# Optimization experiments

Hardware: AMD Instinct MI355X
Metric: run time of the kernel (lower is better)

## Reference

```python
import jax, jax.numpy as jnp
import numpy as np

WS = 7      # window size
NH = 4      # num heads
SHIFT = 3   # cyclic shift

def _rel_index():
    coords = np.stack(np.meshgrid(np.arange(WS), np.arange(WS), indexing='ij')).reshape(2, -1)
    rel = (coords[:, :, None] - coords[:, None, :]).transpose(1, 2, 0).astype(np.int64)
    rel[..., 0] += WS - 1
    rel[..., 1] += WS - 1
    rel[..., 0] *= 2 * WS - 1
    return rel.sum(-1)  # (49, 49)

_REL_IDX = _rel_index()

def _ln(x, g, b):
    mu = x.mean(-1, keepdims=True)
    var = ((x - mu) ** 2).mean(-1, keepdims=True)
    return (x - mu) / jnp.sqrt(var + 1e-5) * g + b

def setup_inputs() -> dict:
    key = jax.random.key(0)
    ks = jax.random.split(key, 8)
    B, H, W, C, HID = 64, 56, 56, 128, 512
    s = 0.02
    return {
        'x': jax.random.normal(ks[0], (B, H * W, C), jnp.float32),
        'norm1_g': jnp.ones((C,), jnp.float32),
        'norm1_b': jnp.zeros((C,), jnp.float32),
        'qkv_w': jax.random.normal(ks[1], (3 * C, C), jnp.float32) * s,
        'qkv_b': jax.random.normal(ks[2], (3 * C,), jnp.float32) * s,
        'proj_w': jax.random.normal(ks[3], (C, C), jnp.float32) * s,
        'proj_b': jax.random.normal(ks[4], (C,), jnp.float32) * s,
        'rpb_table': jax.random.normal(ks[5], ((2 * WS - 1) ** 2, NH), jnp.float32) * s,
        'norm2_g': jnp.ones((C,), jnp.float32),
        'norm2_b': jnp.zeros((C,), jnp.float32),
        'fc1_w': jax.random.normal(ks[6], (HID, C), jnp.float32) * s,
        'fc1_b': jnp.zeros((HID,), jnp.float32),
        'fc2_w': jax.random.normal(ks[7], (C, HID), jnp.float32) * s,
        'fc2_b': jnp.zeros((C,), jnp.float32),
        'H': H,
        'W': W,
    }

def reference(x, norm1_g, norm1_b, qkv_w, qkv_b, proj_w, proj_b, rpb_table,
              norm2_g, norm2_b, fc1_w, fc1_b, fc2_w, fc2_b, H, W):
    B, L, C = x.shape
    hd = C // NH
    scale = hd ** (-0.5)
    shortcut = x
    h = _ln(x, norm1_g, norm1_b).reshape(B, H, W, C)
    pad_h = (-H) % WS
    pad_w = (-W) % WS
    if pad_h or pad_w:
        h = jnp.pad(h, ((0, 0), (0, pad_h), (0, pad_w), (0, 0)))
    Hp, Wp = H + pad_h, W + pad_w
    if SHIFT > 0:
        h = jnp.roll(h, (-SHIFT, -SHIFT), axis=(1, 2))
    # window partition -> (B*nW, 49, C)
    h = h.reshape(B, Hp // WS, WS, Wp // WS, WS, C).transpose(0, 1, 3, 2, 4, 5).reshape(-1, WS * WS, C)
    qkv = h @ qkv_w.T + qkv_b  # (nW, 49, 3C)
    q, k, v = [t.reshape(-1, WS * WS, NH, hd).transpose(0, 2, 1, 3) for t in jnp.split(qkv, 3, axis=-1)]
    attn = jnp.einsum('whnd,whmd->whnm', q * scale, k)  # (nW, NH, 49, 49)
    bias = rpb_table[_REL_IDX.reshape(-1)].reshape(WS * WS, WS * WS, NH).transpose(2, 0, 1)
    attn = jax.nn.softmax(attn + bias[None], axis=-1)
    o = jnp.einsum('whnm,whmd->whnd', attn, v).transpose(0, 2, 1, 3).reshape(-1, WS * WS, C)
    o = o @ proj_w.T + proj_b
    # window reverse -> (B, Hp, Wp, C)
    o = o.reshape(B, Hp // WS, Wp // WS, WS, WS, C).transpose(0, 1, 3, 2, 4, 5).reshape(B, Hp, Wp, C)
    if SHIFT > 0:
        o = jnp.roll(o, (SHIFT, SHIFT), axis=(1, 2))
    o = o[:, :H, :W].reshape(B, H * W, C)
    x = shortcut + o
    h2 = _ln(x, norm2_g, norm2_b)
    h2 = jax.nn.gelu(h2 @ fc1_w.T + fc1_b, approximate=False)
    return x + (h2 @ fc2_w.T + fc2_b)
```

## Files before the change

### kernel.cpp

```cpp
#include <hip/hip_runtime.h>
#include <stdint.h>

static constexpr int Bz   = 64;
static constexpr int HH   = 56, WWp = 56;
static constexpr int C    = 128, HID = 512;
static constexpr int L    = HH * WWp;
static constexpr int M    = Bz * L;
static constexpr int NWIN = Bz * 64;
static constexpr int NH   = 4;
static constexpr int SHIFT = 3;

typedef __bf16 bf16x8 __attribute__((ext_vector_type(8)));
typedef float  f32x4  __attribute__((ext_vector_type(4)));

__device__ __forceinline__ float bf2f(unsigned short u) {
    return __uint_as_float(((unsigned int)u) << 16);
}
__device__ __forceinline__ unsigned short f2bf(float f) {
    unsigned int u = __float_as_uint(f);
    return (unsigned short)((u + 0x7FFFu + ((u >> 16) & 1u)) >> 16);
}
__device__ __forceinline__ unsigned pkbf(float a, float b) {
    unsigned r;
    asm("v_cvt_pk_bf16_f32 %0, %1, %2" : "=v"(r) : "v"(a), "v"(b));
    return r;
}
__device__ __forceinline__ unsigned lds_addr(const void* p) {
    return (unsigned)(size_t)(__attribute__((address_space(3))) const char*)p;
}
__device__ __forceinline__ float gelu_s(float x) {
    float e = __expf(-1.702f * x);
    return x * __builtin_amdgcn_rcpf(1.0f + e);
}

__device__ __forceinline__ int win2orig(int m) {
    int w = m / 49, t = m - w * 49;
    int b = w >> 6, wi = (w >> 3) & 7, wj = w & 7;
    int ti = t / 7, tj = t - ti * 7;
    int i = wi * 7 + ti + SHIFT; if (i >= HH) i -= HH;
    int j = wj * 7 + tj + SHIFT; if (j >= WWp) j -= WWp;
    return b * L + i * WWp + j;
}

__device__ __forceinline__ void async_copy16(void* ldsdst, const void* gsrc) {
    __builtin_amdgcn_global_load_lds(
        (const __attribute__((address_space(1))) unsigned int*)gsrc,
        (__attribute__((address_space(3))) unsigned int*)ldsdst,
        16, 0, 0);
}

__global__ __launch_bounds__(256) void wconv_kernel(
    const float* __restrict__ qkvw, const float* __restrict__ projw,
    const float* __restrict__ fc1w, const float* __restrict__ fc2w,
    const float* __restrict__ rpb, float* __restrict__ biasd,
    unsigned short* __restrict__ wb) {
    int i = blockIdx.x * 256 + threadIdx.x;
    float v;
    if (i < 49152)       v = qkvw[i];
    else if (i < 65536)  v = projw[i - 49152];
    else if (i < 131072) v = fc1w[i - 65536];
    else                 v = fc2w[i - 131072];
    wb[i] = f2bf(v);
    if (i < 16384) {
        int h = i >> 12, l = (i >> 6) & 63, f = i & 63;
        int mi = f >> 4, ni = (f >> 2) & 3, r = f & 3;
        int ii = mi * 16 + (l >> 4) * 4 + r;
        int jj = ni * 16 + (l & 15);
        float bv;
        if (jj >= 49)      bv = -1e30f;
        else if (ii >= 49) bv = 0.f;
        else {
            int yi = ii / 7, xi = ii - yi * 7, yj = jj / 7, xj = jj - yj * 7;
            bv = rpb[((yi - yj + 6) * 13 + (xi - xj + 6)) * NH + h];
        }
        biasd[i] = bv;
    }
}

__global__ __launch_bounds__(256) void ln_kernel(const float* __restrict__ in,
                                                 const float* __restrict__ g,
                                                 const float* __restrict__ bta,
                                                 unsigned short* __restrict__ out) {
    int row  = blockIdx.x * 4 + (threadIdx.x >> 6);
    int lane = threadIdx.x & 63;
    const float2 v = ((const float2*)(in + (long)row * C))[lane];
    float s  = v.x + v.y;
    float ss = v.x * v.x + v.y * v.y;
#pragma unroll
    for (int off = 32; off >= 1; off >>= 1) {
        s  += __shfl_xor(s, off);
        ss += __shfl_xor(ss, off);
    }
    float mu  = s * (1.0f / C);
    float var = ss * (1.0f / C) - mu * mu;
    float rs  = rsqrtf(var + 1e-5f);
    float2 gg = ((const float2*)g)[lane];
    float2 bb = ((const float2*)bta)[lane];
    unsigned o = pkbf((v.x - mu) * rs * gg.x + bb.x,
                      (v.y - mu) * rs * gg.y + bb.y);
    ((unsigned*)(out + (long)row * C))[lane] = o;
}

template<int MODE, int K, int NB, bool GATHER>
__global__ __launch_bounds__(256) void gemm_pipe(
    const unsigned short* __restrict__ A,
    const unsigned short* __restrict__ Wb,
    const float* __restrict__ bias,
    const float* __restrict__ residf,
    const unsigned short* __restrict__ residb,
    const float* __restrict__ g2, const float* __restrict__ b2,
    float* __restrict__ outf,
    unsigned short* __restrict__ outb,
    unsigned short* __restrict__ outb2)
{
    constexpr int KH = K / 64;
    __shared__ char lds[65536];
    char* ldsA = lds;
    char* ldsB = lds + 32768;
    const int tid = threadIdx.x;
    const int wid = tid >> 6, lane = tid & 63;
    const int g = lane >> 4, lr = lane & 15;
    const int wm = wid >> 1, wn = wid & 1;
    const int mbase = blockIdx.x * 128;

    auto stageAfull = [&]() {
#pragma unroll
        for (int i = 0; i < 8; ++i) {
            const int c = i * 4 + wid;
            const int r = (c << 2) + (lane >> 4);
            const int s = (lane & 15) ^ (r & 15);
            long arow = GATHER ? (long)win2orig(mbase + r) : (long)(mbase + r);
            async_copy16(ldsA + c * 1024, (const char*)A + arow * (K * 2) + s * 16);
        }
    };
    auto stageBhalf = [&](int buf, int nb, int kh) {
#pragma unroll
        for (int i = 0; i < 4; ++i) {
            const int c = i * 4 + wid;
            const int r = (c << 3) + (lane >> 3);
            const int s = (lane & 7) ^ (r & 7);
            async_copy16(ldsB + buf * 16384 + c * 1024,
                         (const char*)Wb + (long)(nb * 128 + r) * (K * 2) + kh * 128 + s * 16);
        }
    };

    stageAfull();
    stageBhalf(0, 0, 0);
    __syncthreads();
    int cur = 0;

    for (int nb = 0; nb < NB; ++nb) {
        f32x4 acc[4][4] = {};
        for (int kh = 0; kh < KH; ++kh) {
            const bool last = (nb == NB - 1) && (kh == KH - 1);
            if (!last) {
                const int nnb = (kh == KH - 1) ? nb + 1 : nb;
                const int nkh = (kh == KH - 1) ? 0 : kh + 1;
                stageBhalf(cur ^ 1, nnb, nkh);
            }
#pragma unroll
            for (int kkh = 0; kkh < 2; ++kkh) {
                bf16x8 af[4], bfr[4];
#pragma unroll
                for (int mi = 0; mi < 4; ++mi) {
                    const int ra = wm * 64 + mi * 16 + lr;
                    const int kk = kh * 2 + kkh;
                    af[mi] = *(const bf16x8*)(ldsA + ra * 256 + (((kk * 4 + g) ^ (ra & 15)) * 16));
                }
#pragma unroll
                for (int ni = 0; ni < 4; ++ni) {
                    const int rb = wn * 64 + ni * 16 + lr;
                    bfr[ni] = *(const bf16x8*)(ldsB + cur * 16384 + rb * 128 + (((kkh * 4 + g) ^ (rb & 7)) * 16));
                }
#pragma unroll
                for (int mi = 0; mi < 4; ++mi)
#pragma unroll
                    for (int ni = 0; ni < 4; ++ni)
                        acc[mi][ni] = __builtin_amdgcn_mfma_f32_16x16x32_bf16(bfr[ni], af[mi], acc[mi][ni], 0, 0, 0);
            }
            if (!last) { __syncthreads(); cur ^= 1; }
        }

        int rr[4];
#pragma unroll
        for (int mi = 0; mi < 4; ++mi)
            rr[mi] = win2orig(mbase + wm * 64 + mi * 16 + lr);
#pragma unroll
        for (int mi = 0; mi < 4; ++mi)
#pragma unroll
            for (int ni = 0; ni < 4; ++ni) {
                const int nloc = wn * 64 + ni * 16 + g * 4;
                const f32x4 b4 = *(const f32x4*)&bias[nloc];
                const f32x4 r4 = *(const f32x4*)&residf[(long)rr[mi] * C + nloc];
                acc[mi][ni] += b4 + r4;
            }
        float sA[4], qA[4];
#pragma unroll
        for (int mi = 0; mi < 4; ++mi) {
            float s = 0.f, q = 0.f;
#pragma unroll
            for (int ni = 0; ni < 4; ++ni)
#pragma unroll
                for (int rg = 0; rg < 4; ++rg) {
                    float v = acc[mi][ni][rg];
                    s += v; q += v * v;
                }
            s += __shfl_xor(s, 16); q += __shfl_xor(q, 16);
            s += __shfl_xor(s, 32); q += __shfl_xor(q, 32);
            sA[mi] = s; qA[mi] = q;
        }
        float* lp = (float*)lds;
        __syncthreads();
        if (g == 0) {
#pragma unroll
            for (int mi = 0; mi < 4; ++mi) {
                int r64 = mi * 16 + lr;
                lp[((wm * 64 + r64) * 2 + wn) * 2 + 0] = sA[mi];
                lp[((wm * 64 + r64) * 2 + wn) * 2 + 1] = qA[mi];
            }
        }
        __syncthreads();
#pragma unroll
        for (int mi = 0; mi < 4; ++mi) {
            const int r64 = mi * 16 + lr;
            const float st = sA[mi] + lp[((wm * 64 + r64) * 2 + (wn ^ 1)) * 2 + 0];
            const float qt = qA[mi] + lp[((wm * 64 + r64) * 2 + (wn ^ 1)) * 2 + 1];
            const float mu = st * (1.0f / C);
            const float var = qt * (1.0f / C) - mu * mu;
            const float rs = rsqrtf(var + 1e-5f);
            const long rbase = (long)rr[mi] * C;
#pragma unroll
            for (int ni = 0; ni < 4; ++ni) {
                const int nloc = wn * 64 + ni * 16 + g * 4;
                float xv[4], hv[4];
#pragma unroll
                for (int rg = 0; rg < 4; ++rg) {
                    xv[rg] = acc[mi][ni][rg];
                    hv[rg] = (xv[rg] - mu) * rs * g2[nloc + rg] + b2[nloc + rg];
                }
                *(uint2*)(outb2 + rbase + nloc) = make_uint2(pkbf(xv[0], xv[1]), pkbf(xv[2], xv[3]));
                *(uint2*)(outb  + rbase + nloc) = make_uint2(pkbf(hv[0], hv[1]), pkbf(hv[2], hv[3]));
            }
        }
    }
}

__global__ __launch_bounds__(256, 3) void qkv_attn(
    const unsigned short* __restrict__ hn,
    const unsigned short* __restrict__ Wqkv,
    const float* __restrict__ qvb,
    const float* __restrict__ biasd,
    unsigned short* __restrict__ ob)
{
    __shared__ __align__(16) char reg1[16384];
    __shared__ __align__(16) char reg2[32768];
    const int tid  = threadIdx.x;
    const int h    = tid >> 6;
    const int lane = tid & 63;
    const int g    = lane >> 4, lr = lane & 15;
    const int w    = blockIdx.x;

#pragma unroll
    for (int rnd = 0; rnd < 4; ++rnd) {
        const int cb  = rnd * 4 + h;
        const int row = cb * 4 + g;
        const int t   = (row < 49) ? row : row - 49;
        const int s   = lr ^ (row & 15);
        const long ar = win2orig(w * 49 + t);
        async_copy16(reg1 + cb * 1024, (const char*)hn + ar * 256 + s * 16);
    }
    __syncthreads();

    const unsigned short* Wq = Wqkv + (long)(h * 32) * 128;
    const unsigned short* Wk = Wqkv + (long)(128 + h * 32) * 128;
    f32x4 aqk[4][4] = {};
#pragma unroll
    for (int kk = 0; kk < 4; ++kk) {
        bf16x8 af[4], wf[4];
#pragma unroll
        for (int mi = 0; mi < 4; ++mi)
            af[mi] = *(const bf16x8*)(reg1 + (mi * 16 + lr) * 256 + (((kk * 4 + g) ^ lr) * 16));
        wf[0] = *(const bf16x8*)(Wq + (long)lr * 128 + kk * 32 + g * 8);
        wf[1] = *(const bf16x8*)(Wq + (long)(16 + lr) * 128 + kk * 32 + g * 8);
        wf[2] = *(const bf16x8*)(Wk + (long)lr * 128 + kk * 32 + g * 8);
        wf[3] = *(const bf16x8*)(Wk + (long)(16 + lr) * 128 + kk * 32 + g * 8);
#pragma unroll
        for (int nf = 0; nf < 4; ++nf)
#pragma unroll
            for (int mi = 0; mi < 4; ++mi)
                aqk[nf][mi] = __builtin_amdgcn_mfma_f32_16x16x32_bf16(wf[nf], af[mi], aqk[nf][mi], 0, 0, 0);
    }
    char* qlds = reg2 + h * 8192;
    char* klds = qlds + 4096;
    const float scale = 0.17677669529663687f;
#pragma unroll
    for (int nf = 0; nf < 4; ++nf) {
        const bool isq = (nf < 2);
        const int d0 = (nf & 1) * 16 + g * 4;
        const f32x4 b4 = *(const f32x4*)&qvb[(isq ? 0 : 128) + h * 32 + d0];
        char* dst = isq ? qlds : klds;
#pragma unroll
        for (int mi = 0; mi < 4; ++mi) {
            const int t = mi * 16 + lr;
            float v0 = aqk[nf][mi][0] + b4[0], v1 = aqk[nf][mi][1] + b4[1];
            float v2 = aqk[nf][mi][2] + b4[2], v3 = aqk[nf][mi][3] + b4[3];
            if (isq) { v0 *= scale; v1 *= scale; v2 *= scale; v3 *= scale; }
            *(uint2*)(dst + t * 64 + d0 * 2) = make_uint2(pkbf(v0, v1), pkbf(v2, v3));
        }
    }

    const unsigned short* Wv = Wqkv + (long)(256 + h * 32) * 128;
    f32x4 av[2][4] = {};
#pragma unroll
    for (int kk = 0; kk < 4; ++kk) {
        bf16x8 af[4], wf[2];
#pragma unroll
        for (int mi = 0; mi < 4; ++mi)
            af[mi] = *(const bf16x8*)(reg1 + (mi * 16 + lr) * 256 + (((kk * 4 + g) ^ lr) * 16));
        wf[0] = *(const bf16x8*)(Wv + (long)lr * 128 + kk * 32 + g * 8);
        wf[1] = *(const bf16x8*)(Wv + (long)(16 + lr) * 128 + kk * 32 + g * 8);
#pragma unroll
        for (int nf = 0; nf < 2; ++nf)
#pragma unroll
            for (int mi = 0; mi < 4; ++mi)
                av[nf][mi] = __builtin_amdgcn_mfma_f32_16x16x32_bf16(af[mi], wf[nf], av[nf][mi], 0, 0, 0);
    }
    __syncthreads();
    char* vlds = reg1 + h * 4096;
#pragma unroll
    for (int nf = 0; nf < 2; ++nf) {
        const int d = nf * 16 + lr;
        const float bv = qvb[256 + h * 32 + d];
#pragma unroll
        for (int mi = 0; mi < 4; ++mi) {
            const int t0 = mi * 16 + g * 4;
            const int slot = t0 >> 3;
            *(uint2*)(vlds + d * 128 + ((slot ^ (d & 7)) * 16) + (g & 1) * 8) =
                make_uint2(pkbf(av[nf][mi][0] + bv, av[nf][mi][1] + bv),
                           pkbf(av[nf][mi][2] + bv, av[nf][mi][3] + bv));
        }
    }

    bf16x8 qf[4], kf[4];
#pragma unroll
    for (int mi = 0; mi < 4; ++mi) {
        qf[mi] = *(const bf16x8*)(qlds + (mi * 16 + lr) * 64 + g * 16);
        kf[mi] = *(const bf16x8*)(klds + (mi * 16 + lr) * 64 + g * 16);
    }
    f32x4 acc[4][4] = {};
#pragma unroll
    for (int mi = 0; mi < 4; ++mi)
#pragma unroll
        for (int ni = 0; ni < 4; ++ni)
            acc[mi][ni] = __builtin_amdgcn_mfma_f32_16x16x32_bf16(qf[mi], kf[ni], acc[mi][ni], 0, 0, 0);

    const float* bp = biasd + (h * 64 + lane) * 64;
    char* ptw = reg2 + h * 8192;
#pragma unroll
    for (int mi = 0; mi < 4; ++mi) {
#pragma unroll
        for (int ni = 0; ni < 4; ++ni)
            acc[mi][ni] += *(const f32x4*)(bp + mi * 16 + ni * 4);
#pragma unroll
        for (int c = 0; c < 4; ++c)
            acc[mi][3][c] = (lr == 0) ? acc[mi][3][c] : -1e30f;
        f32x4 mx;
#pragma unroll
        for (int c = 0; c < 4; ++c)
            mx[c] = fmaxf(fmaxf(acc[mi][0][c], acc[mi][1][c]), fmaxf(acc[mi][2][c], acc[mi][3][c]));
#pragma unroll
        for (int off = 1; off <= 8; off <<= 1)
#pragma unroll
            for (int c = 0; c < 4; ++c)
                mx[c] = fmaxf(mx[c], __shfl_xor(mx[c], off));
        f32x4 sum = {};
#pragma unroll
        for (int ni = 0; ni < 4; ++ni)
#pragma unroll
            for (int c = 0; c < 4; ++c) {
                float e = __expf(acc[mi][ni][c] - mx[c]);
                acc[mi][ni][c] = e;
                sum[c] += e;
            }
#pragma unroll
        for (int off = 1; off <= 8; off <<= 1)
#pragma unroll
            for (int c = 0; c < 4; ++c)
                sum[c] += __shfl_xor(sum[c], off);
        f32x4 inv;
#pragma unroll
        for (int c = 0; c < 4; ++c)
            inv[c] = __builtin_amdgcn_rcpf(sum[c]);
#pragma unroll
        for (int ni = 0; ni < 4; ++ni) {
            int jb  = ni * 4 + (lr >> 2);
            int tix = (((jb >> 3) * 2 + (jb & 1)) * 4 + mi) * 4 + ((jb >> 1) & 3);
            *(uint2*)(ptw + tix * 128 + (lr & 3) * 32 + g * 8) =
                make_uint2(pkbf(acc[mi][ni][0] * inv[0], acc[mi][ni][1] * inv[1]),
                           pkbf(acc[mi][ni][2] * inv[2], acc[mi][ni][3] * inv[3]));
        }
    }
    asm volatile("s_waitcnt lgkmcnt(0)" ::: "memory");

    bf16x8 vf[2][2];
#pragma unroll
    for (int md = 0; md < 2; ++md)
#pragma unroll
        for (int kk = 0; kk < 2; ++kk)
            vf[md][kk] = *(const bf16x8*)(vlds + (md * 16 + lr) * 128 + (((kk * 4 + g) ^ (lr & 7)) * 16));

    const unsigned pbase = lds_addr(ptw);
    f32x4 accO[2][4] = {};
#pragma unroll
    for (int kk = 0; kk < 2; ++kk) {
        long tt[4][2];
#pragma unroll
        for (int ni = 0; ni < 4; ++ni)
#pragma unroll
            for (int s = 0; s < 2; ++s) {
                unsigned a = pbase + ((((kk * 2 + s) * 4 + ni) * 4 + g) * 128) + lr * 2;
                asm volatile("ds_read_b64_tr_b16 %0, %1" : "=v"(tt[ni][s]) : "v"(a));
            }
        asm volatile("s_waitcnt lgkmcnt(0)" ::: "memory");
        __builtin_amdgcn_sched_barrier(0);
#pragma unroll
        for (int ni = 0; ni < 4; ++ni) {
            union { int4 i4; bf16x8 v; } u;
            u.i4 = make_int4((int)tt[ni][0], (int)(tt[ni][0] >> 32),
                             (int)tt[ni][1], (int)(tt[ni][1] >> 32));
#pragma unroll
            for (int md = 0; md < 2; ++md)
                accO[md][ni] = __builtin_amdgcn_mfma_f32_16x16x32_bf16(vf[md][kk], u.v, accO[md][ni], 0, 0, 0);
        }
    }
#pragma unroll
    for (int ni = 0; ni < 4; ++ni) {
        int i = ni * 16 + lr;
        if (i < 49) {
#pragma unroll
            for (int md = 0; md < 2; ++md) {
                *(uint2*)(ob + ((long)(w * 49 + i)) * 128 + h * 32 + md * 16 + g * 4) =
                    make_uint2(pkbf(accO[md][ni][0], accO[md][ni][1]),
                               pkbf(accO[md][ni][2], accO[md][ni][3]));
            }
        }
    }
}

__global__ __launch_bounds__(256, 4) void mlp_fused(
    const unsigned short* __restrict__ A,
    const unsigned short* __restrict__ W1,
    const unsigned short* __restrict__ W2,
    const float* __restrict__ b1,
    const float* __restrict__ b2,
    const unsigned short* __restrict__ resid,
    float* __restrict__ out)
{
    __shared__ char ldsW[16384];
    __shared__ char ldsP[8192];
    const int tid = threadIdx.x;
    const int wid = tid >> 6, lane = tid & 63;
    const int g = lane >> 4, lr = lane & 15;
    const int wm = wid >> 1, wn = wid & 1;
    const int mbase = blockIdx.x * 64;

    bf16x8 af[2][4];
#pragma unroll
    for (int mi = 0; mi < 2; ++mi) {
        const long rb = (long)(mbase + wm * 32 + mi * 16 + lr) * 128;
#pragma unroll
        for (int kk = 0; kk < 4; ++kk)
            af[mi][kk] = *(const bf16x8*)(A + rb + kk * 32 + g * 8);
    }

    auto stageW1 = [&](int c) {
#pragma unroll
        for (int i = 0; i < 4; ++i) {
            const int cb = i * 4 + wid;
            const int r  = cb * 4 + g;
            const int s  = lr ^ (r & 15);
            async_copy16(ldsW + cb * 1024, (const char*)W1 + (long)(c * 64 + r) * 256 + s * 16);
        }
    };

    stageW1(0);
    f32x4 oacc[2][4] = {};

    for (int c = 0; c < 8; ++c) {
        __syncthreads();
        f32x4 pacc[2][2] = {};
#pragma unroll
        for (int kk = 0; kk < 4; ++kk) {
            bf16x8 w1f[2];
#pragma unroll
            for (int ni = 0; ni < 2; ++ni) {
                const int rb = wn * 32 + ni * 16 + lr;
                w1f[ni] = *(const bf16x8*)(ldsW + rb * 256 + (((kk * 4 + g) ^ (rb & 15)) * 16));
            }
#pragma unroll
            for (int mi = 0; mi < 2; ++mi)
#pragma unroll
                for (int ni = 0; ni < 2; ++ni)
                    pacc[mi][ni] = __builtin_amdgcn_mfma_f32_16x16x32_bf16(w1f[ni], af[mi][kk], pacc[mi][ni], 0, 0, 0);
        }
#pragma unroll
        for (int mi = 0; mi < 2; ++mi) {
            const int m = wm * 32 + mi * 16 + lr;
#pragma unroll
            for (int ni = 0; ni < 2; ++ni) {
                const int h0 = wn * 32 + ni * 16 + g * 4;
                const f32x4 b4 = *(const f32x4*)&b1[c * 64 + h0];
                const int slot = h0 >> 3;
                *(uint2*)(ldsP + m * 128 + ((slot ^ (m & 7)) * 16) + (g & 1) * 8) =
                    make_uint2(pkbf(gelu_s(pacc[mi][ni][0] + b4[0]), gelu_s(pacc[mi][ni][1] + b4[1])),
                               pkbf(gelu_s(pacc[mi][ni][2] + b4[2]), gelu_s(pacc[mi][ni][3] + b4[3])));
            }
        }
        __syncthreads();
        if (c < 7) stageW1(c + 1);
#pragma unroll
        for (int kk = 0; kk < 2; ++kk) {
            bf16x8 pf[2], w2f[4];
#pragma unroll
            for (int mi = 0; mi < 2; ++mi) {
                const int ra = wm * 32 + mi * 16 + lr;
                pf[mi] = *(const bf16x8*)(ldsP + ra * 128 + (((kk * 4 + g) ^ (ra & 7)) * 16));
            }
#pragma unroll
            for (int ni = 0; ni < 4; ++ni)
                w2f[ni] = *(const bf16x8*)(W2 + (long)(wn * 64 + ni * 16 + lr) * 512 + c * 64 + kk * 32 + g * 8);
#pragma unroll
            for (int mi = 0; mi < 2; ++mi)
#pragma unroll
                for (int ni = 0; ni < 4; ++ni)
                    oacc[mi][ni] = __builtin_amdgcn_mfma_f32_16x16x32_bf16(w2f[ni], pf[mi], oacc[mi][ni], 0, 0, 0);
        }
    }

#pragma unroll
    for (int mi = 0; mi < 2; ++mi) {
        const long gm = mbase + wm * 32 + mi * 16 + lr;
#pragma unroll
        for (int ni = 0; ni < 4; ++ni) {
            const int n0 = wn * 64 + ni * 16 + g * 4;
            const f32x4 b4 = *(const f32x4*)&b2[n0];
            const ushort4 r4 = *(const ushort4*)(resid + gm * C + n0);
            f32x4 o4;
            o4[0] = oacc[mi][ni][0] + b4[0] + bf2f(r4.x);
            o4[1] = oacc[mi][ni][1] + b4[1] + bf2f(r4.y);
            o4[2] = oacc[mi][ni][2] + b4[2] + bf2f(r4.z);
            o4[3] = oacc[mi][ni][3] + b4[3] + bf2f(r4.w);
            *(f32x4*)(out + gm * C + n0) = o4;
        }
    }
}

extern "C" void kernel_launch(void* const* d_in, const int* in_sizes, int n_in,
                              void* d_out, int out_size, void* d_ws, size_t ws_size,
                              hipStream_t stream) {
    const float* x      = (const float*)d_in[0];
    const float* n1g    = (const float*)d_in[1];
    const float* n1b    = (const float*)d_in[2];
    const float* qkv_w  = (const float*)d_in[3];
    const float* qkv_b  = (const float*)d_in[4];
    const float* proj_w = (const float*)d_in[5];
    const float* proj_b = (const float*)d_in[6];
    const float* rpb    = (const float*)d_in[7];
    const float* n2g    = (const float*)d_in[8];
    const float* n2b    = (const float*)d_in[9];
    const float* fc1_w  = (const float*)d_in[10];
    const float* fc1_b  = (const float*)d_in[11];
    const float* fc2_w  = (const float*)d_in[12];
    const float* fc2_b  = (const float*)d_in[13];
    float* out = (float*)d_out;

    char* ws = (char*)d_ws;
    const size_t SZ = (size_t)M * C * 2;
    unsigned short* hnorm = (unsigned short*)(ws);
    unsigned short* o     = (unsigned short*)(ws + SZ);
    unsigned short* x2b   = (unsigned short*)(ws + 2 * SZ);
    unsigned short* h2n   = (unsigned short*)(ws + 3 * SZ);
    unsigned short* wb    = (unsigned short*)(ws + 4 * SZ);
    float* biasd          = (float*)(ws + 4 * SZ + 393216);
    unsigned short* wqkv = wb, *wproj = wb + 49152, *wfc1 = wb + 65536, *wfc2 = wb + 131072;

    wconv_kernel<<<768, 256, 0, stream>>>(qkv_w, proj_w, fc1_w, fc2_w, rpb, biasd, wb);
    ln_kernel<<<M / 4, 256, 0, stream>>>(x, n1g, n1b, hnorm);
    qkv_attn<<<NWIN, 256, 0, stream>>>(hnorm, wqkv, qkv_b, biasd, o);
    gemm_pipe<1, 128, 1, false><<<M / 128, 256, 0, stream>>>(o, wproj, proj_b, x, nullptr, n2g, n2b, nullptr, h2n, x2b);
    mlp_fused<<<M / 64, 256, 0, stream>>>(h2n, wfc1, wfc2, fc1_b, fc2_b, x2b, out);
}
```

Baseline: 378.2 us.

## Make fused MLP warp-independent with per-wave rows and no block barriers

Restructures the fused MLP kernel so each wave owns 16 rows and computes all 64 hidden columns per chunk and all 128 output columns, instead of a 2x2 wave grid sharing tiles. W1 is now read straight from global memory (through cache) rather than staged in shared memory with async copies. The GELU intermediate goes to a per-wave, double-buffered shared-memory slot, so all block-wide __syncthreads are removed. The trade-off is more global/L2 weight traffic per wave (each wave reloads the full W1 and W2 chunk) and more accumulator registers, in exchange for eliminating barrier stalls.

```diff
diff --git a/kernel.cpp b/kernel.cpp
--- a/kernel.cpp
+++ b/kernel.cpp
@@ -456,102 +456,66 @@
     const unsigned short* __restrict__ resid,
     float* __restrict__ out)
 {
-    __shared__ char ldsW[16384];
-    __shared__ char ldsP[8192];
+    __shared__ __align__(16) char ldsP[4][2][2048];
     const int tid = threadIdx.x;
     const int wid = tid >> 6, lane = tid & 63;
     const int g = lane >> 4, lr = lane & 15;
-    const int wm = wid >> 1, wn = wid & 1;
-    const int mbase = blockIdx.x * 64;
-
-    bf16x8 af[2][4];
-#pragma unroll
-    for (int mi = 0; mi < 2; ++mi) {
-        const long rb = (long)(mbase + wm * 32 + mi * 16 + lr) * 128;
-#pragma unroll
-        for (int kk = 0; kk < 4; ++kk)
-            af[mi][kk] = *(const bf16x8*)(A + rb + kk * 32 + g * 8);
-    }
-
-    auto stageW1 = [&](int c) {
-#pragma unroll
-        for (int i = 0; i < 4; ++i) {
-            const int cb = i * 4 + wid;
-            const int r  = cb * 4 + g;
-            const int s  = lr ^ (r & 15);
-            async_copy16(ldsW + cb * 1024, (const char*)W1 + (long)(c * 64 + r) * 256 + s * 16);
-        }
-    };
-
-    stageW1(0);
-    f32x4 oacc[2][4] = {};
+    const int row0 = blockIdx.x * 64 + wid * 16;
+
+    bf16x8 af[4];
+#pragma unroll
+    for (int kk = 0; kk < 4; ++kk)
+        af[kk] = *(const bf16x8*)(A + (long)(row0 + lr) * 128 + kk * 32 + g * 8);
+
+    f32x4 oacc[8] = {};
 
     for (int c = 0; c < 8; ++c) {
-        __syncthreads();
-        f32x4 pacc[2][2] = {};
+        char* P = ldsP[wid][c & 1];
+        f32x4 pacc[4] = {};
 #pragma unroll
         for (int kk = 0; kk < 4; ++kk) {
-            bf16x8 w1f[2];
-#pragma unroll
-            for (int ni = 0; ni < 2; ++ni) {
-                const int rb = wn * 32 + ni * 16 + lr;
-                w1f[ni] = *(const bf16x8*)(ldsW + rb * 256 + (((kk * 4 + g) ^ (rb & 15)) * 16));
-            }
-#pragma unroll
-            for (int mi = 0; mi < 2; ++mi)
-#pragma unroll
-                for (int ni = 0; ni < 2; ++ni)
-                    pacc[mi][ni] = __builtin_amdgcn_mfma_f32_16x16x32_bf16(w1f[ni], af[mi][kk], pacc[mi][ni], 0, 0, 0);
-        }
-#pragma unroll
-        for (int mi = 0; mi < 2; ++mi) {
-            const int m = wm * 32 + mi * 16 + lr;
-#pragma unroll
-            for (int ni = 0; ni < 2; ++ni) {
-                const int h0 = wn * 32 + ni * 16 + g * 4;
-                const f32x4 b4 = *(const f32x4*)&b1[c * 64 + h0];
-                const int slot = h0 >> 3;
-                *(uint2*)(ldsP + m * 128 + ((slot ^ (m & 7)) * 16) + (g & 1) * 8) =
-                    make_uint2(pkbf(gelu_s(pacc[mi][ni][0] + b4[0]), gelu_s(pacc[mi][ni][1] + b4[1])),
-                               pkbf(gelu_s(pacc[mi][ni][2] + b4[2]), gelu_s(pacc[mi][ni][3] + b4[3])));
-            }
-        }
-        __syncthreads();
-        if (c < 7) stageW1(c + 1);
+            bf16x8 w1f[4];
+#pragma unroll
+            for (int ni = 0; ni < 4; ++ni)
+                w1f[ni] = *(const bf16x8*)(W1 + (long)(c * 64 + ni * 16 + lr) * 128 + kk * 32 + g * 8);
+#pragma unroll
+            for (int ni = 0; ni < 4; ++ni)
+                pacc[ni] = __builtin_amdgcn_mfma_f32_16x16x32_bf16(w1f[ni], af[kk], pacc[ni], 0, 0, 0);
+        }
+#pragma unroll
+        for (int ni = 0; ni < 4; ++ni) {
+            const int h0 = ni * 16 + g * 4;
+            const f32x4 b4 = *(const f32x4*)&b1[c * 64 + h0];
+            const int slot = h0 >> 3;
+            *(uint2*)(P + lr * 128 + ((slot ^ (lr & 7)) * 16) + (g & 1) * 8) =
+                make_uint2(pkbf(gelu_s(pacc[0 + ni][0] + b4[0]), gelu_s(pacc[ni][1] + b4[1])),
+                           pkbf(gelu_s(pacc[ni][2] + b4[2]), gelu_s(pacc[ni][3] + b4[3])));
+        }
 #pragma unroll
         for (int kk = 0; kk < 2; ++kk) {
-            bf16x8 pf[2], w2f[4];
-#pragma unroll
-            for (int mi = 0; mi < 2; ++mi) {
-                const int ra = wm * 32 + mi * 16 + lr;
-                pf[mi] = *(const bf16x8*)(ldsP + ra * 128 + (((kk * 4 + g) ^ (ra & 7)) * 16));
-            }
-#pragma unroll
-            for (int ni = 0; ni < 4; ++ni)
-                w2f[ni] = *(const bf16x8*)(W2 + (long)(wn * 64 + ni * 16 + lr) * 512 + c * 64 + kk * 32 + g * 8);
-#pragma unroll
-            for (int mi = 0; mi < 2; ++mi)
-#pragma unroll
-                for (int ni = 0; ni < 4; ++ni)
-                    oacc[mi][ni] = __builtin_amdgcn_mfma_f32_16x16x32_bf16(w2f[ni], pf[mi], oacc[mi][ni], 0, 0, 0);
-        }
-    }
-
-#pragma unroll
-    for (int mi = 0; mi < 2; ++mi) {
-        const long gm = mbase + wm * 32 + mi * 16 + lr;
-#pragma unroll
-        for (int ni = 0; ni < 4; ++ni) {
-            const int n0 = wn * 64 + ni * 16 + g * 4;
-            const f32x4 b4 = *(const f32x4*)&b2[n0];
-            const ushort4 r4 = *(const ushort4*)(resid + gm * C + n0);
-            f32x4 o4;
-            o4[0] = oacc[mi][ni][0] + b4[0] + bf2f(r4.x);
-            o4[1] = oacc[mi][ni][1] + b4[1] + bf2f(r4.y);
-            o4[2] = oacc[mi][ni][2] + b4[2] + bf2f(r4.z);
-            o4[3] = oacc[mi][ni][3] + b4[3] + bf2f(r4.w);
-            *(f32x4*)(out + gm * C + n0) = o4;
-        }
+            const bf16x8 pf = *(const bf16x8*)(P + lr * 128 + (((kk * 4 + g) ^ (lr & 7)) * 16));
+            bf16x8 w2f[8];
+#pragma unroll
+            for (int ni = 0; ni < 8; ++ni)
+                w2f[ni] = *(const bf16x8*)(W2 + (long)(ni * 16 + lr) * 512 + c * 64 + kk * 32 + g * 8);
+#pragma unroll
+            for (int ni = 0; ni < 8; ++ni)
+                oacc[ni] = __builtin_amdgcn_mfma_f32_16x16x32_bf16(w2f[ni], pf, oacc[ni], 0, 0, 0);
+        }
+    }
+
+#pragma unroll
+    for (int ni = 0; ni < 8; ++ni) {
+        const int n0 = ni * 16 + g * 4;
+        const long gm = row0 + lr;
+        const f32x4 b4 = *(const f32x4*)&b2[n0];
+        const ushort4 r4 = *(const ushort4*)(resid + gm * C + n0);
+        f32x4 o4;
+        o4[0] = oacc[ni][0] + b4[0] + bf2f(r4.x);
+        o4[1] = oacc[ni][1] + b4[1] + bf2f(r4.y);
+        o4[2] = oacc[ni][2] + b4[2] + bf2f(r4.z);
+        o4[3] = oacc[ni][3] + b4[3] + bf2f(r4.w);
+        *(f32x4*)(out + gm * C + n0) = o4;
     }
 }
 
```

Measured after the change: 637.7 us. 68.6% more time.
